# Optimization experiments

Measured on AMD Instinct MI355X. Metric: run time of the kernel, lower is better.

The kernel has to match this reference:

```python
import jax, jax.numpy as jnp
import numpy as np

B, S, D, H = 8, 128, 256, 8
T = S + 1
HD = D // H  # head_dim = 32
GAMMA = 1.0
NEG_INF = -1e9
LN_EPS = 1e-5


def setup_inputs() -> dict:
    key = jax.random.key(0)
    ks = jax.random.split(key, 16)
    sc = 0.05
    return {
        "desc_embeddings": jax.random.normal(ks[0], (B, S, D), jnp.float32),
        "name_value_embeddings": jax.random.normal(ks[1], (B, T, D), jnp.float32),
        "prior_Q": jax.random.uniform(ks[2], (B, H, S, S), jnp.float32),
        "Wq": jax.random.normal(ks[3], (D, D), jnp.float32) * sc,
        "bq": jnp.zeros((D,), jnp.float32),
        "Wk": jax.random.normal(ks[4], (D, D), jnp.float32) * sc,
        "bk": jnp.zeros((D,), jnp.float32),
        "Wv": jax.random.normal(ks[5], (D, D), jnp.float32) * sc,
        "bv": jnp.zeros((D,), jnp.float32),
        "wa": jax.random.normal(ks[6], (3 * HD,), jnp.float32) * sc,  # attn_proj weight (out=1)
        "ba": jnp.zeros((), jnp.float32),
        "We1": jax.random.normal(ks[7], (2 * D, D), jnp.float32) * sc,
        "be1": jnp.zeros((D,), jnp.float32),
        "ln_g": jnp.ones((D,), jnp.float32),
        "ln_b": jnp.zeros((D,), jnp.float32),
        "We2": jax.random.normal(ks[8], (D, D), jnp.float32) * sc,
        "be2": jnp.zeros((D,), jnp.float32),
    }


def _layer_norm(x, g, b):
    mu = jnp.mean(x, axis=-1, keepdims=True)
    var = jnp.mean(jnp.square(x - mu), axis=-1, keepdims=True)
    return (x - mu) * jax.lax.rsqrt(var + LN_EPS) * g + b


def _heads(x, W, b):  # [B,T,D] -> [B,H,T,HD]
    return (x @ W + b).reshape(B, T, H, HD).transpose(0, 2, 1, 3)


def reference(desc_embeddings, name_value_embeddings, prior_Q,
              Wq, bq, Wk, bk, Wv, bv, wa, ba,
              We1, be1, ln_g, ln_b, We2, be2):
    # structural adjacency (same for every batch element): CLS->Var on, Var->CLS off,
    # Var-Var fully connected without self-loops
    adj = jnp.zeros((T, T), jnp.float32)
    adj = adj.at[1:, 1:].set(1.0 - jnp.eye(S, dtype=jnp.float32))
    adj = adj.at[0, 1:].set(1.0)

    q = _heads(name_value_embeddings, Wq, bq)  # [B,H,T,HD]
    k = _heads(name_value_embeddings, Wk, bk)
    v = _heads(name_value_embeddings, Wv, bv)

    # edge attributes: pairwise concat of desc embeddings, CLS rows/cols use [desc,desc]
    desc = desc_embeddings
    var_edge = jnp.concatenate([
        jnp.broadcast_to(desc[:, :, None, :], (B, S, S, D)),
        jnp.broadcast_to(desc[:, None, :, :], (B, S, S, D)),
    ], axis=-1)  # [B,S,S,2D]
    cls_edge = jnp.concatenate([desc, desc], axis=-1)  # [B,S,2D]
    edge = jnp.zeros((B, T, T, 2 * D), jnp.float32)
    edge = edge.at[:, 1:, 1:].set(var_edge)
    edge = edge.at[:, 0, 1:].set(cls_edge)
    edge = edge.at[:, 1:, 0].set(cls_edge)

    # edge_update MLP: Linear(2D->D) -> LayerNorm -> ReLU -> Linear(D->D)
    h = jax.nn.relu(_layer_norm(edge @ We1 + be1, ln_g, ln_b)) @ We2 + be2  # [B,T,T,D]
    # split into heads, mask by adjacency: [B,H,T,T,HD]
    edge_h = h.reshape(B, T, T, H, HD).transpose(0, 3, 1, 2, 4)
    edge_h = edge_h * adj[None, None, :, :, None]

    # gat_v1 + attn_proj(cat[q_i, k_j, e_ij]) is linear -> decompose to avoid
    # materializing the [B,H,T,T,3*HD] concat
    wa_q, wa_k, wa_e = wa[:HD], wa[HD:2 * HD], wa[2 * HD:]
    logits = (jnp.einsum('bhid,d->bhi', q, wa_q)[:, :, :, None]
              + jnp.einsum('bhjd,d->bhj', k, wa_k)[:, :, None, :]
              + jnp.einsum('bhijd,d->bhij', edge_h, wa_e)
              + ba)  # [B,H,T,T]

    # prior_Q logit-bias injection on Var-Var block
    eps = 1e-6
    p = jnp.clip(prior_Q, eps, 1.0 - eps)
    bias = (jnp.log(p) - jnp.log(1.0 - p)) * GAMMA  # [B,H,S,S]
    logits = logits.at[:, :, 1:, 1:].add(bias)

    # structural mask as pre-softmax -inf
    logits = logits + (adj == 0).astype(logits.dtype)[None, None] * NEG_INF

    attn = jax.nn.softmax(logits, axis=-1)  # [B,H,T,T]
    ctx = jnp.einsum('bhij,bhjd->bhid', attn, v)  # [B,H,T,HD]
    basis_outputs = ctx.transpose(0, 2, 1, 3)  # [B,T,H,HD]
    return basis_outputs, attn
```

## Files before the change

### kernel.cpp

```cpp
#include <hip/hip_runtime.h>
#include <math.h>

#define B 8
#define S 128
#define D 256
#define H 8
#define T 129
#define HD 32
#define NEG_INF -1000000000.0f
#define LN_EPS 1e-5f

__global__ __launch_bounds__(256) void prep_w(
    const float* __restrict__ Wq, const float* __restrict__ bq,
    const float* __restrict__ Wk, const float* __restrict__ bk,
    const float* __restrict__ We2, const float* __restrict__ be2,
    const float* __restrict__ wa,
    float* __restrict__ Wqk, float* __restrict__ bqk,
    float* __restrict__ W2aT, float* __restrict__ econst)
{
    int id = blockIdx.x * 256 + threadIdx.x;
    if (id < 2048) {
        int c = id >> 3, h = id & 7;
        float s = 0.f;
        #pragma unroll
        for (int d = 0; d < HD; ++d) s = fmaf(Wq[c*D + h*HD + d], wa[d], s);
        Wqk[c*16 + h] = s;
    } else if (id < 4096) {
        int id2 = id - 2048; int c = id2 >> 3, h = id2 & 7;
        float s = 0.f;
        #pragma unroll
        for (int d = 0; d < HD; ++d) s = fmaf(Wk[c*D + h*HD + d], wa[HD + d], s);
        Wqk[c*16 + 8 + h] = s;
    } else if (id < 6144) {
        int id2 = id - 4096; int h = id2 / D, c = id2 % D;
        float s = 0.f;
        #pragma unroll
        for (int d = 0; d < HD; ++d) s = fmaf(We2[c*D + h*HD + d], wa[2*HD + d], s);
        W2aT[h*D + c] = s;
    } else if (id < 6152) {
        int h = id - 6144;
        float s = 0.f;
        #pragma unroll
        for (int d = 0; d < HD; ++d) s = fmaf(bq[h*HD + d], wa[d], s);
        bqk[h] = s;
    } else if (id < 6160) {
        int h = id - 6152;
        float s = 0.f;
        #pragma unroll
        for (int d = 0; d < HD; ++d) s = fmaf(bk[h*HD + d], wa[HD + d], s);
        bqk[8 + h] = s;
    } else if (id < 6168) {
        int h = id - 6160;
        float s = 0.f;
        #pragma unroll
        for (int d = 0; d < HD; ++d) s = fmaf(be2[h*HD + d], wa[2*HD + d], s);
        econst[h] = s;
    }
}

__global__ __launch_bounds__(256) void gemm3(
    const float* __restrict__ nv, const float* __restrict__ desc,
    const float* __restrict__ Wv, const float* __restrict__ bv,
    const float* __restrict__ We1, const float* __restrict__ be1,
    float* __restrict__ v, float* __restrict__ U, float* __restrict__ V)
{
    const int which = blockIdx.y;
    const float* X; const float* W; const float* bias; float* out; int rows;
    if (which == 0)      { X = nv;   W = Wv;        bias = bv;  out = v; rows = B*T; }
    else if (which == 1) { X = desc; W = We1;       bias = be1; out = U; rows = B*S; }
    else                 { X = desc; W = We1 + D*D; bias = nullptr; out = V; rows = B*S; }

    const int r0  = blockIdx.x * 8;
    const int tid = threadIdx.x;
    __shared__ float xs[8][D];

    #pragma unroll
    for (int r = 0; r < 8; ++r) {
        int rr = r0 + r;
        xs[r][tid] = (rr < rows) ? X[rr * D + tid] : 0.f;
    }
    __syncthreads();

    float acc[8] = {0.f,0.f,0.f,0.f,0.f,0.f,0.f,0.f};
    for (int kk = 0; kk < D; kk += 4) {
        float w0 = W[(kk+0)*D + tid];
        float w1 = W[(kk+1)*D + tid];
        float w2 = W[(kk+2)*D + tid];
        float w3 = W[(kk+3)*D + tid];
        #pragma unroll
        for (int r = 0; r < 8; ++r) {
            float4 x = *(const float4*)&xs[r][kk];
            acc[r] = fmaf(x.x, w0, acc[r]);
            acc[r] = fmaf(x.y, w1, acc[r]);
            acc[r] = fmaf(x.z, w2, acc[r]);
            acc[r] = fmaf(x.w, w3, acc[r]);
        }
    }
    const float bb = bias ? bias[tid] : 0.f;
    #pragma unroll
    for (int r = 0; r < 8; ++r) {
        int rr = r0 + r;
        if (rr < rows) out[rr * D + tid] = acc[r] + bb;
    }
}

__global__ __launch_bounds__(256) void qdkd_gemm(
    const float* __restrict__ nv, const float* __restrict__ Wqk,
    const float* __restrict__ bqk, float* __restrict__ qdkd)
{
    const int r0 = blockIdx.x * 16;
    const int tid = threadIdx.x;
    const int r = tid >> 4, c = tid & 15;
    __shared__ float xs[16][D];

    for (int t = tid; t < 16 * D; t += 256) {
        int rr = r0 + (t >> 8);
        xs[t >> 8][t & 255] = (rr < B*T) ? nv[rr * D + (t & 255)] : 0.f;
    }
    __syncthreads();

    float acc = 0.f;
    for (int kk = 0; kk < D; kk += 4) {
        float4 x = *(const float4*)&xs[r][kk];
        acc = fmaf(x.x, Wqk[(kk+0)*16 + c], acc);
        acc = fmaf(x.y, Wqk[(kk+1)*16 + c], acc);
        acc = fmaf(x.z, Wqk[(kk+2)*16 + c], acc);
        acc = fmaf(x.w, Wqk[(kk+3)*16 + c], acc);
    }
    const int rr = r0 + r;
    if (rr < B*T) qdkd[rr * 16 + c] = acc + bqk[c];
}

__global__ __launch_bounds__(512) void edge_attn(
    const float* __restrict__ U, const float* __restrict__ V,
    const float* __restrict__ W2aT, const float* __restrict__ econst,
    const float* __restrict__ ln_g, const float* __restrict__ ln_b,
    const float* __restrict__ qdkd, const float* __restrict__ prior,
    const float* __restrict__ v, const float* __restrict__ ba,
    float* __restrict__ out_basis, float* __restrict__ out_attn)
{
    const int bid = blockIdx.x;
    const int b = bid / T, i = bid % T;
    const int tid = threadIdx.x, lane = tid & 63, wid = tid >> 6;
    const int c0 = lane * 4;

    __shared__ float escl[H][132];
    __shared__ float pat[H][132];

    const float4 g4 = *(const float4*)(ln_g + c0);
    const float4 b4 = *(const float4*)(ln_b + c0);
    float4 w[H];
    #pragma unroll
    for (int h = 0; h < H; ++h) w[h] = *(const float4*)(W2aT + h*D + c0);
    float4 u4i = make_float4(0.f, 0.f, 0.f, 0.f);
    if (i >= 1) u4i = *(const float4*)(U + (b*S + (i-1))*D + c0);

    const int hmap = 4*(lane&1) + 2*((lane>>1)&1) + ((lane>>2)&1);
    const float ecl = (lane < 8) ? econst[hmap] : 0.f;

    const int j0 = 1 + wid * 16;
    for (int jj = 0; jj < 16; ++jj) {
        const int j = j0 + jj;
        if (i >= 1 && j == i) continue;

        const float4 v4 = *(const float4*)(V + (b*S + (j-1))*D + c0);
        float4 u4;
        if (i == 0) u4 = *(const float4*)(U + (b*S + (j-1))*D + c0);
        else        u4 = u4i;

        const float y0 = u4.x + v4.x, y1 = u4.y + v4.y;
        const float y2 = u4.z + v4.z, y3 = u4.w + v4.w;

        float s1 = y0 + y1 + y2 + y3;
        float s2 = fmaf(y0, y0, fmaf(y1, y1, fmaf(y2, y2, y3 * y3)));
        #pragma unroll
        for (int m = 32; m >= 1; m >>= 1) {
            s1 += __shfl_xor(s1, m);
            s2 += __shfl_xor(s2, m);
        }
        const float mu  = s1 * (1.f / D);
        const float var = s2 * (1.f / D) - mu * mu;
        const float rs  = rsqrtf(var + LN_EPS);

        const float t0 = fmaxf((y0 - mu) * rs * g4.x + b4.x, 0.f);
        const float t1 = fmaxf((y1 - mu) * rs * g4.y + b4.y, 0.f);
        const float t2 = fmaxf((y2 - mu) * rs * g4.z + b4.z, 0.f);
        const float t3 = fmaxf((y3 - mu) * rs * g4.w + b4.w, 0.f);

        float ph[H];
        #pragma unroll
        for (int h = 0; h < H; ++h)
            ph[h] = fmaf(t0, w[h].x, fmaf(t1, w[h].y, fmaf(t2, w[h].z, t3 * w[h].w)));

        {
            const bool hi = (lane & 1);
            float k0 = hi ? ph[4] : ph[0], d0 = hi ? ph[0] : ph[4];
            float k1 = hi ? ph[5] : ph[1], d1 = hi ? ph[1] : ph[5];
            float k2 = hi ? ph[6] : ph[2], d2 = hi ? ph[2] : ph[6];
            float k3 = hi ? ph[7] : ph[3], d3 = hi ? ph[3] : ph[7];
            ph[0] = k0 + __shfl_xor(d0, 1);
            ph[1] = k1 + __shfl_xor(d1, 1);
            ph[2] = k2 + __shfl_xor(d2, 1);
            ph[3] = k3 + __shfl_xor(d3, 1);
        }
        {
            const bool hi = (lane & 2);
            float k0 = hi ? ph[2] : ph[0], d0 = hi ? ph[0] : ph[2];
            float k1 = hi ? ph[3] : ph[1], d1 = hi ? ph[1] : ph[3];
            ph[0] = k0 + __shfl_xor(d0, 2);
            ph[1] = k1 + __shfl_xor(d1, 2);
        }
        {
            const bool hi = (lane & 4);
            float k0 = hi ? ph[1] : ph[0], d0 = hi ? ph[0] : ph[1];
            ph[0] = k0 + __shfl_xor(d0, 4);
        }
        ph[0] += __shfl_xor(ph[0], 8);
        ph[0] += __shfl_xor(ph[0], 16);
        ph[0] += __shfl_xor(ph[0], 32);

        if (lane < 8) escl[hmap][j] = ph[0] + ecl;
    }
    __syncthreads();

    const int h = wid;
    const int bh = b*H + h;
    const float qdv = qdkd[(b*T + i)*16 + h];
    const float ba0 = ba[0];
    const int j1 = 1 + lane, j2 = 65 + lane;
    const bool v1 = !(i >= 1 && j1 == i);
    const bool v2 = !(i >= 1 && j2 == i);

    float l1 = NEG_INF, l2 = NEG_INF;
    if (v1) {
        l1 = qdv + qdkd[(b*T + j1)*16 + 8 + h] + escl[h][j1] + ba0;
        if (i >= 1) {
            float pr = prior[(bh*S + (i-1))*S + (j1-1)];
            pr = fminf(fmaxf(pr, 1e-6f), 1.f - 1e-6f);
            l1 += logf(pr) - logf(1.f - pr);
        }
    }
    if (v2) {
        l2 = qdv + qdkd[(b*T + j2)*16 + 8 + h] + escl[h][j2] + ba0;
        if (i >= 1) {
            float pr = prior[(bh*S + (i-1))*S + (j2-1)];
            pr = fminf(fmaxf(pr, 1e-6f), 1.f - 1e-6f);
            l2 += logf(pr) - logf(1.f - pr);
        }
    }

    float m = fmaxf(l1, l2);
    #pragma unroll
    for (int mm = 32; mm >= 1; mm >>= 1) m = fmaxf(m, __shfl_xor(m, mm));
    const float e1 = v1 ? expf(l1 - m) : 0.f;
    const float e2 = v2 ? expf(l2 - m) : 0.f;
    float s = e1 + e2;
    #pragma unroll
    for (int mm = 32; mm >= 1; mm >>= 1) s += __shfl_xor(s, mm);
    const float inv = 1.f / s;
    const float a1 = e1 * inv, a2 = e2 * inv;

    float* arow = out_attn + (size_t)(bh*T + i)*T;
    arow[j1] = a1;
    arow[j2] = a2;
    if (lane == 0) arow[0] = 0.f;
    pat[h][j1] = a1;
    pat[h][j2] = a2;
    __syncthreads();

    const int d = lane & 31, half = lane >> 5;
    float acc = 0.f;
    const float* vb = v + (size_t)(b*T)*D + h*HD + d;
    #pragma unroll 4
    for (int jj = 0; jj < 64; ++jj) {
        const int j = 1 + half*64 + jj;
        acc = fmaf(pat[h][j], vb[j*D], acc);
    }
    acc += __shfl_xor(acc, 32);
    if (lane < 32)
        out_basis[((b*T + i)*H + h)*HD + d] = acc;
}

extern "C" void kernel_launch(void* const* d_in, const int* in_sizes, int n_in,
                              void* d_out, int out_size, void* d_ws, size_t ws_size,
                              hipStream_t stream) {
    const float* desc  = (const float*)d_in[0];
    const float* nv    = (const float*)d_in[1];
    const float* prior = (const float*)d_in[2];
    const float* Wq  = (const float*)d_in[3];
    const float* bq  = (const float*)d_in[4];
    const float* Wk  = (const float*)d_in[5];
    const float* bk  = (const float*)d_in[6];
    const float* Wv  = (const float*)d_in[7];
    const float* bv  = (const float*)d_in[8];
    const float* wa  = (const float*)d_in[9];
    const float* ba  = (const float*)d_in[10];
    const float* We1 = (const float*)d_in[11];
    const float* be1 = (const float*)d_in[12];
    const float* lng = (const float*)d_in[13];
    const float* lnb = (const float*)d_in[14];
    const float* We2 = (const float*)d_in[15];
    const float* be2 = (const float*)d_in[16];

    float* ws = (float*)d_ws;
    float* U    = ws; ws += B*S*D;
    float* V    = ws; ws += B*S*D;
    float* v    = ws; ws += B*T*D;
    float* Wqk  = ws; ws += D*16;
    float* bqk  = ws; ws += 16;
    float* W2aT = ws; ws += H*D;
    float* ec   = ws; ws += H;
    float* qdkd = ws; ws += B*T*16;

    float* out_basis = (float*)d_out;
    float* out_attn  = out_basis + B*T*H*HD;

    prep_w<<<dim3(25), 256, 0, stream>>>(Wq, bq, Wk, bk, We2, be2, wa,
                                         Wqk, bqk, W2aT, ec);
    gemm3<<<dim3(129, 3), 256, 0, stream>>>(nv, desc, Wv, bv, We1, be1, v, U, V);
    qdkd_gemm<<<dim3(65), 256, 0, stream>>>(nv, Wqk, bqk, qdkd);
    edge_attn<<<dim3(B*T), 512, 0, stream>>>(U, V, W2aT, ec, lng, lnb,
                                             qdkd, prior, v, ba,
                                             out_basis, out_attn);
}
```

Baseline: 174.3 us.

## Fuse qdkd GEMM into gemm3, precompute row sums, unroll edge loop, vectorize ctx

Folds the separate q/k score GEMM into the gemm3 launch as a fourth grid slice, removing one kernel launch. It also precomputes the U and V row sums so the LayerNorm mean needs no cross-lane reduction. The edge loop now handles two j values per iteration to overlap shuffle latency, and the context product uses float4 loads of v. Fast __logf/__expf intrinsics, a transposed qdkd layout and launch bounds of 4 blocks are added, which trade some precision and register headroom.

New measurement: 159.9 us. 8.2% less time.

```diff
diff --git a/kernel.cpp b/kernel.cpp
--- a/kernel.cpp
+++ b/kernel.cpp
@@ -7,6 +7,7 @@
 #define H 8
 #define T 129
 #define HD 32
+#define BT (B*T)
 #define NEG_INF -1000000000.0f
 #define LN_EPS 1e-5f
 
@@ -62,17 +63,44 @@
     const float* __restrict__ nv, const float* __restrict__ desc,
     const float* __restrict__ Wv, const float* __restrict__ bv,
     const float* __restrict__ We1, const float* __restrict__ be1,
-    float* __restrict__ v, float* __restrict__ U, float* __restrict__ V)
+    const float* __restrict__ Wqk, const float* __restrict__ bqk,
+    float* __restrict__ v, float* __restrict__ U, float* __restrict__ V,
+    float* __restrict__ sU, float* __restrict__ sV, float* __restrict__ qdkdT)
 {
     const int which = blockIdx.y;
+    const int tid = threadIdx.x;
+    __shared__ float xs[16][D];
+    __shared__ float psum[4][8];
+
+    if (which == 3) {
+        if (blockIdx.x >= 65) return;
+        const int r0 = blockIdx.x * 16;
+        const int r = tid >> 4, c = tid & 15;
+        for (int t = tid; t < 16 * D; t += 256) {
+            int rr = r0 + (t >> 8);
+            xs[t >> 8][t & 255] = (rr < BT) ? nv[rr * D + (t & 255)] : 0.f;
+        }
+        __syncthreads();
+        float acc = 0.f;
+        for (int kk = 0; kk < D; kk += 4) {
+            float4 x = *(const float4*)&xs[r][kk];
+            acc = fmaf(x.x, Wqk[(kk+0)*16 + c], acc);
+            acc = fmaf(x.y, Wqk[(kk+1)*16 + c], acc);
+            acc = fmaf(x.z, Wqk[(kk+2)*16 + c], acc);
+            acc = fmaf(x.w, Wqk[(kk+3)*16 + c], acc);
+        }
+        const int rr = r0 + r;
+        if (rr < BT) qdkdT[c*BT + rr] = acc + bqk[c];
+        return;
+    }
+
     const float* X; const float* W; const float* bias; float* out; int rows;
-    if (which == 0)      { X = nv;   W = Wv;        bias = bv;  out = v; rows = B*T; }
+    if (which == 0)      { X = nv;   W = Wv;        bias = bv;  out = v; rows = BT; }
     else if (which == 1) { X = desc; W = We1;       bias = be1; out = U; rows = B*S; }
     else                 { X = desc; W = We1 + D*D; bias = nullptr; out = V; rows = B*S; }
 
-    const int r0  = blockIdx.x * 8;
-    const int tid = threadIdx.x;
-    __shared__ float xs[8][D];
+    const int r0 = blockIdx.x * 8;
+    if (r0 >= rows) return;
 
     #pragma unroll
     for (int r = 0; r < 8; ++r) {
@@ -102,41 +130,62 @@
         int rr = r0 + r;
         if (rr < rows) out[rr * D + tid] = acc[r] + bb;
     }
-}
-
-__global__ __launch_bounds__(256) void qdkd_gemm(
-    const float* __restrict__ nv, const float* __restrict__ Wqk,
-    const float* __restrict__ bqk, float* __restrict__ qdkd)
-{
-    const int r0 = blockIdx.x * 16;
-    const int tid = threadIdx.x;
-    const int r = tid >> 4, c = tid & 15;
-    __shared__ float xs[16][D];
-
-    for (int t = tid; t < 16 * D; t += 256) {
-        int rr = r0 + (t >> 8);
-        xs[t >> 8][t & 255] = (rr < B*T) ? nv[rr * D + (t & 255)] : 0.f;
-    }
-    __syncthreads();
-
-    float acc = 0.f;
-    for (int kk = 0; kk < D; kk += 4) {
-        float4 x = *(const float4*)&xs[r][kk];
-        acc = fmaf(x.x, Wqk[(kk+0)*16 + c], acc);
-        acc = fmaf(x.y, Wqk[(kk+1)*16 + c], acc);
-        acc = fmaf(x.z, Wqk[(kk+2)*16 + c], acc);
-        acc = fmaf(x.w, Wqk[(kk+3)*16 + c], acc);
-    }
-    const int rr = r0 + r;
-    if (rr < B*T) qdkd[rr * 16 + c] = acc + bqk[c];
-}
-
-__global__ __launch_bounds__(512) void edge_attn(
+
+    if (which >= 1) {
+        const int wv = tid >> 6, ln = tid & 63;
+        #pragma unroll
+        for (int r = 0; r < 8; ++r) {
+            float sps = acc[r] + bb;
+            #pragma unroll
+            for (int m = 32; m >= 1; m >>= 1) sps += __shfl_xor(sps, m);
+            if (ln == 0) psum[wv][r] = sps;
+        }
+        __syncthreads();
+        if (tid < 8) {
+            float* dst = (which == 1) ? sU : sV;
+            dst[r0 + tid] = psum[0][tid] + psum[1][tid] + psum[2][tid] + psum[3][tid];
+        }
+    }
+}
+
+__device__ __forceinline__ float head_reduce(float* ph, int lane) {
+    {
+        const bool hi = (lane & 1);
+        float k0 = hi ? ph[4] : ph[0], d0 = hi ? ph[0] : ph[4];
+        float k1 = hi ? ph[5] : ph[1], d1 = hi ? ph[1] : ph[5];
+        float k2 = hi ? ph[6] : ph[2], d2 = hi ? ph[2] : ph[6];
+        float k3 = hi ? ph[7] : ph[3], d3 = hi ? ph[3] : ph[7];
+        ph[0] = k0 + __shfl_xor(d0, 1);
+        ph[1] = k1 + __shfl_xor(d1, 1);
+        ph[2] = k2 + __shfl_xor(d2, 1);
+        ph[3] = k3 + __shfl_xor(d3, 1);
+    }
+    {
+        const bool hi = (lane & 2);
+        float k0 = hi ? ph[2] : ph[0], d0 = hi ? ph[0] : ph[2];
+        float k1 = hi ? ph[3] : ph[1], d1 = hi ? ph[1] : ph[3];
+        ph[0] = k0 + __shfl_xor(d0, 2);
+        ph[1] = k1 + __shfl_xor(d1, 2);
+    }
+    {
+        const bool hi = (lane & 4);
+        float k0 = hi ? ph[1] : ph[0], d0 = hi ? ph[0] : ph[1];
+        ph[0] = k0 + __shfl_xor(d0, 4);
+    }
+    float r = ph[0];
+    r += __shfl_xor(r, 8);
+    r += __shfl_xor(r, 16);
+    r += __shfl_xor(r, 32);
+    return r;
+}
+
+__global__ __launch_bounds__(512, 4) void edge_attn(
     const float* __restrict__ U, const float* __restrict__ V,
     const float* __restrict__ W2aT, const float* __restrict__ econst,
     const float* __restrict__ ln_g, const float* __restrict__ ln_b,
-    const float* __restrict__ qdkd, const float* __restrict__ prior,
+    const float* __restrict__ qdkdT, const float* __restrict__ prior,
     const float* __restrict__ v, const float* __restrict__ ba,
+    const float* __restrict__ sU, const float* __restrict__ sV,
     float* __restrict__ out_basis, float* __restrict__ out_attn)
 {
     const int bid = blockIdx.x;
@@ -152,112 +201,114 @@
     float4 w[H];
     #pragma unroll
     for (int h = 0; h < H; ++h) w[h] = *(const float4*)(W2aT + h*D + c0);
+
     float4 u4i = make_float4(0.f, 0.f, 0.f, 0.f);
-    if (i >= 1) u4i = *(const float4*)(U + (b*S + (i-1))*D + c0);
+    float sUi = 0.f;
+    if (i >= 1) {
+        u4i = *(const float4*)(U + (size_t)(b*S + (i-1))*D + c0);
+        sUi = sU[b*S + (i-1)];
+    }
 
     const int hmap = 4*(lane&1) + 2*((lane>>1)&1) + ((lane>>2)&1);
     const float ecl = (lane < 8) ? econst[hmap] : 0.f;
 
     const int j0 = 1 + wid * 16;
-    for (int jj = 0; jj < 16; ++jj) {
-        const int j = j0 + jj;
-        if (i >= 1 && j == i) continue;
-
-        const float4 v4 = *(const float4*)(V + (b*S + (j-1))*D + c0);
-        float4 u4;
-        if (i == 0) u4 = *(const float4*)(U + (b*S + (j-1))*D + c0);
-        else        u4 = u4i;
-
-        const float y0 = u4.x + v4.x, y1 = u4.y + v4.y;
-        const float y2 = u4.z + v4.z, y3 = u4.w + v4.w;
-
-        float s1 = y0 + y1 + y2 + y3;
-        float s2 = fmaf(y0, y0, fmaf(y1, y1, fmaf(y2, y2, y3 * y3)));
+    const float* Vb  = V  + (size_t)(b*S + (j0-1))*D + c0;
+    const float* Ub  = U  + (size_t)(b*S + (j0-1))*D + c0;
+    const float* sVb = sV + b*S + (j0-1);
+    const float* sUb = sU + b*S + (j0-1);
+
+    #pragma unroll 2
+    for (int jj = 0; jj < 16; jj += 2) {
+        const float4 va  = *(const float4*)(Vb + (size_t)jj*D);
+        const float4 vb4 = *(const float4*)(Vb + (size_t)(jj+1)*D);
+        float4 ua, ub; float su_a, su_b;
+        if (i == 0) {
+            ua = *(const float4*)(Ub + (size_t)jj*D);
+            ub = *(const float4*)(Ub + (size_t)(jj+1)*D);
+            su_a = sUb[jj]; su_b = sUb[jj+1];
+        } else { ua = u4i; ub = u4i; su_a = sUi; su_b = sUi; }
+
+        const float mua = (su_a + sVb[jj])   * (1.f/D);
+        const float mub = (su_b + sVb[jj+1]) * (1.f/D);
+
+        const float ya0 = ua.x + va.x,  ya1 = ua.y + va.y;
+        const float ya2 = ua.z + va.z,  ya3 = ua.w + va.w;
+        const float yb0 = ub.x + vb4.x, yb1 = ub.y + vb4.y;
+        const float yb2 = ub.z + vb4.z, yb3 = ub.w + vb4.w;
+
+        float s2a = fmaf(ya0, ya0, fmaf(ya1, ya1, fmaf(ya2, ya2, ya3 * ya3)));
+        float s2b = fmaf(yb0, yb0, fmaf(yb1, yb1, fmaf(yb2, yb2, yb3 * yb3)));
         #pragma unroll
         for (int m = 32; m >= 1; m >>= 1) {
-            s1 += __shfl_xor(s1, m);
-            s2 += __shfl_xor(s2, m);
-        }
-        const float mu  = s1 * (1.f / D);
-        const float var = s2 * (1.f / D) - mu * mu;
-        const float rs  = rsqrtf(var + LN_EPS);
-
-        const float t0 = fmaxf((y0 - mu) * rs * g4.x + b4.x, 0.f);
-        const float t1 = fmaxf((y1 - mu) * rs * g4.y + b4.y, 0.f);
-        const float t2 = fmaxf((y2 - mu) * rs * g4.z + b4.z, 0.f);
-        const float t3 = fmaxf((y3 - mu) * rs * g4.w + b4.w, 0.f);
-
-        float ph[H];
-        #pragma unroll
-        for (int h = 0; h < H; ++h)
-            ph[h] = fmaf(t0, w[h].x, fmaf(t1, w[h].y, fmaf(t2, w[h].z, t3 * w[h].w)));
-
-        {
-            const bool hi = (lane & 1);
-            float k0 = hi ? ph[4] : ph[0], d0 = hi ? ph[0] : ph[4];
-            float k1 = hi ? ph[5] : ph[1], d1 = hi ? ph[1] : ph[5];
-            float k2 = hi ? ph[6] : ph[2], d2 = hi ? ph[2] : ph[6];
-            float k3 = hi ? ph[7] : ph[3], d3 = hi ? ph[3] : ph[7];
-            ph[0] = k0 + __shfl_xor(d0, 1);
-            ph[1] = k1 + __shfl_xor(d1, 1);
-            ph[2] = k2 + __shfl_xor(d2, 1);
-            ph[3] = k3 + __shfl_xor(d3, 1);
-        }
-        {
-            const bool hi = (lane & 2);
-            float k0 = hi ? ph[2] : ph[0], d0 = hi ? ph[0] : ph[2];
-            float k1 = hi ? ph[3] : ph[1], d1 = hi ? ph[1] : ph[3];
-            ph[0] = k0 + __shfl_xor(d0, 2);
-            ph[1] = k1 + __shfl_xor(d1, 2);
-        }
-        {
-            const bool hi = (lane & 4);
-            float k0 = hi ? ph[1] : ph[0], d0 = hi ? ph[0] : ph[1];
-            ph[0] = k0 + __shfl_xor(d0, 4);
-        }
-        ph[0] += __shfl_xor(ph[0], 8);
-        ph[0] += __shfl_xor(ph[0], 16);
-        ph[0] += __shfl_xor(ph[0], 32);
-
-        if (lane < 8) escl[hmap][j] = ph[0] + ecl;
+            s2a += __shfl_xor(s2a, m);
+            s2b += __shfl_xor(s2b, m);
+        }
+        const float vara = fmaf(-mua, mua, s2a * (1.f/D));
+        const float varb = fmaf(-mub, mub, s2b * (1.f/D));
+        const float rsa = rsqrtf(vara + LN_EPS);
+        const float rsb = rsqrtf(varb + LN_EPS);
+
+        const float ta0 = fmaxf(fmaf((ya0 - mua) * rsa, g4.x, b4.x), 0.f);
+        const float ta1 = fmaxf(fmaf((ya1 - mua) * rsa, g4.y, b4.y), 0.f);
+        const float ta2 = fmaxf(fmaf((ya2 - mua) * rsa, g4.z, b4.z), 0.f);
+        const float ta3 = fmaxf(fmaf((ya3 - mua) * rsa, g4.w, b4.w), 0.f);
+        const float tb0 = fmaxf(fmaf((yb0 - mub) * rsb, g4.x, b4.x), 0.f);
+        const float tb1 = fmaxf(fmaf((yb1 - mub) * rsb, g4.y, b4.y), 0.f);
+        const float tb2 = fmaxf(fmaf((yb2 - mub) * rsb, g4.z, b4.z), 0.f);
+        const float tb3 = fmaxf(fmaf((yb3 - mub) * rsb, g4.w, b4.w), 0.f);
+
+        float pha[8], phb[8];
+        #pragma unroll
+        for (int h = 0; h < H; ++h) {
+            pha[h] = fmaf(ta0, w[h].x, fmaf(ta1, w[h].y, fmaf(ta2, w[h].z, ta3 * w[h].w)));
+            phb[h] = fmaf(tb0, w[h].x, fmaf(tb1, w[h].y, fmaf(tb2, w[h].z, tb3 * w[h].w)));
+        }
+        const float ra = head_reduce(pha, lane);
+        const float rb = head_reduce(phb, lane);
+        if (lane < 8) {
+            escl[hmap][j0 + jj]     = ra + ecl;
+            escl[hmap][j0 + jj + 1] = rb + ecl;
+        }
     }
     __syncthreads();
 
     const int h = wid;
     const int bh = b*H + h;
-    const float qdv = qdkd[(b*T + i)*16 + h];
+    const float qdv = qdkdT[h*BT + b*T + i];
     const float ba0 = ba[0];
     const int j1 = 1 + lane, j2 = 65 + lane;
-    const bool v1 = !(i >= 1 && j1 == i);
-    const bool v2 = !(i >= 1 && j2 == i);
+    const bool val1 = !(i >= 1 && j1 == i);
+    const bool val2 = !(i >= 1 && j2 == i);
+    const float* kT = qdkdT + (8 + h)*BT + b*T;
 
     float l1 = NEG_INF, l2 = NEG_INF;
-    if (v1) {
-        l1 = qdv + qdkd[(b*T + j1)*16 + 8 + h] + escl[h][j1] + ba0;
+    if (val1) {
+        l1 = qdv + kT[j1] + escl[h][j1] + ba0;
         if (i >= 1) {
-            float pr = prior[(bh*S + (i-1))*S + (j1-1)];
+            float pr = prior[((size_t)bh*S + (i-1))*S + (j1-1)];
             pr = fminf(fmaxf(pr, 1e-6f), 1.f - 1e-6f);
-            l1 += logf(pr) - logf(1.f - pr);
-        }
-    }
-    if (v2) {
-        l2 = qdv + qdkd[(b*T + j2)*16 + 8 + h] + escl[h][j2] + ba0;
+            l1 += __logf(pr) - __logf(1.f - pr);
+        }
+    }
+    if (val2) {
+        l2 = qdv + kT[j2] + escl[h][j2] + ba0;
         if (i >= 1) {
-            float pr = prior[(bh*S + (i-1))*S + (j2-1)];
+            float pr = prior[((size_t)bh*S + (i-1))*S + (j2-1)];
             pr = fminf(fmaxf(pr, 1e-6f), 1.f - 1e-6f);
-            l2 += logf(pr) - logf(1.f - pr);
+            l2 += __logf(pr) - __logf(1.f - pr);
         }
     }
 
     float m = fmaxf(l1, l2);
     #pragma unroll
     for (int mm = 32; mm >= 1; mm >>= 1) m = fmaxf(m, __shfl_xor(m, mm));
-    const float e1 = v1 ? expf(l1 - m) : 0.f;
-    const float e2 = v2 ? expf(l2 - m) : 0.f;
-    float s = e1 + e2;
-    #pragma unroll
-    for (int mm = 32; mm >= 1; mm >>= 1) s += __shfl_xor(s, mm);
-    const float inv = 1.f / s;
+    const float e1 = val1 ? __expf(l1 - m) : 0.f;
+    const float e2 = val2 ? __expf(l2 - m) : 0.f;
+    float ssum = e1 + e2;
+    #pragma unroll
+    for (int mm = 32; mm >= 1; mm >>= 1) ssum += __shfl_xor(ssum, mm);
+    const float inv = 1.f / ssum;
     const float a1 = e1 * inv, a2 = e2 * inv;
 
     float* arow = out_attn + (size_t)(bh*T + i)*T;
@@ -268,17 +319,29 @@
     pat[h][j2] = a2;
     __syncthreads();
 
-    const int d = lane & 31, half = lane >> 5;
-    float acc = 0.f;
-    const float* vb = v + (size_t)(b*T)*D + h*HD + d;
-    #pragma unroll 4
-    for (int jj = 0; jj < 64; ++jj) {
-        const int j = 1 + half*64 + jj;
-        acc = fmaf(pat[h][j], vb[j*D], acc);
-    }
-    acc += __shfl_xor(acc, 32);
-    if (lane < 32)
-        out_basis[((b*T + i)*H + h)*HD + d] = acc;
+    const int dg = lane & 7;
+    const int jg = lane >> 3;
+    const float* vbase = v + (size_t)(b*T)*D + h*HD + dg*4;
+    float4 acc4 = make_float4(0.f, 0.f, 0.f, 0.f);
+    #pragma unroll
+    for (int k = 0; k < 16; ++k) {
+        const int j = 1 + jg*16 + k;
+        const float p = pat[h][j];
+        const float4 vv = *(const float4*)(vbase + (size_t)j*D);
+        acc4.x = fmaf(p, vv.x, acc4.x);
+        acc4.y = fmaf(p, vv.y, acc4.y);
+        acc4.z = fmaf(p, vv.z, acc4.z);
+        acc4.w = fmaf(p, vv.w, acc4.w);
+    }
+    #pragma unroll
+    for (int mm = 8; mm <= 32; mm <<= 1) {
+        acc4.x += __shfl_xor(acc4.x, mm);
+        acc4.y += __shfl_xor(acc4.y, mm);
+        acc4.z += __shfl_xor(acc4.z, mm);
+        acc4.w += __shfl_xor(acc4.w, mm);
+    }
+    if (jg == 0)
+        *(float4*)(out_basis + ((size_t)(b*T + i)*H + h)*HD + dg*4) = acc4;
 }
 
 extern "C" void kernel_launch(void* const* d_in, const int* in_sizes, int n_in,
@@ -303,23 +366,25 @@
     const float* be2 = (const float*)d_in[16];
 
     float* ws = (float*)d_ws;
-    float* U    = ws; ws += B*S*D;
-    float* V    = ws; ws += B*S*D;
-    float* v    = ws; ws += B*T*D;
-    float* Wqk  = ws; ws += D*16;
-    float* bqk  = ws; ws += 16;
-    float* W2aT = ws; ws += H*D;
-    float* ec   = ws; ws += H;
-    float* qdkd = ws; ws += B*T*16;
+    float* U     = ws; ws += B*S*D;
+    float* V     = ws; ws += B*S*D;
+    float* v     = ws; ws += B*T*D;
+    float* Wqk   = ws; ws += D*16;
+    float* bqk   = ws; ws += 16;
+    float* W2aT  = ws; ws += H*D;
+    float* ec    = ws; ws += H;
+    float* qdkdT = ws; ws += 16*BT;
+    float* sU    = ws; ws += B*S;
+    float* sV    = ws; ws += B*S;
 
     float* out_basis = (float*)d_out;
     float* out_attn  = out_basis + B*T*H*HD;
 
     prep_w<<<dim3(25), 256, 0, stream>>>(Wq, bq, Wk, bk, We2, be2, wa,
                                          Wqk, bqk, W2aT, ec);
-    gemm3<<<dim3(129, 3), 256, 0, stream>>>(nv, desc, Wv, bv, We1, be1, v, U, V);
-    qdkd_gemm<<<dim3(65), 256, 0, stream>>>(nv, Wqk, bqk, qdkd);
+    gemm3<<<dim3(129, 4), 256, 0, stream>>>(nv, desc, Wv, bv, We1, be1,
+                                            Wqk, bqk, v, U, V, sU, sV, qdkdT);
     edge_attn<<<dim3(B*T), 512, 0, stream>>>(U, V, W2aT, ec, lng, lnb,
-                                             qdkd, prior, v, ba,
+                                             qdkdT, prior, v, ba, sU, sV,
                                              out_basis, out_attn);
 }
```
